# Kernel optimization log

Measured on AMD Instinct MI355X. Metric: run time of the kernel, lower is better.

Reference implementation:

```python
import jax, jax.numpy as jnp
import numpy as np

N_NODES = 10000
N_EDGES = 50000
N_GRAPHS = 64
NODE_DIM = 32
EDGE_DIM = 16
HID = 64
EDGE_HID = 128
OUT_DIM = 1
T_STEPS = 3       # message-passing rounds
S2S_STEPS = 6     # Set2Set processing steps


def setup_inputs() -> dict:
    key = jax.random.key(0)
    ks = jax.random.split(key, 24)
    def w(k, shape, scale):
        return (jax.random.normal(k, shape, dtype=jnp.float32) * scale)
    inp = {}
    inp["node_features"] = jax.random.normal(ks[0], (N_NODES, NODE_DIM), dtype=jnp.float32)
    inp["edge_features"] = jax.random.normal(ks[1], (N_EDGES, EDGE_DIM), dtype=jnp.float32)
    inp["edge_index"] = jax.random.randint(ks[2], (2, N_EDGES), 0, N_NODES, dtype=jnp.int32)
    # sorted, fully-covering graph assignment (nodes of each graph are contiguous)
    inp["batch_indices"] = ((jnp.arange(N_NODES) * N_GRAPHS) // N_NODES).astype(jnp.int32)
    # input projection
    inp["W_proj"] = w(ks[3], (NODE_DIM, HID), 1.0 / np.sqrt(NODE_DIM))
    inp["b_proj"] = jnp.zeros((HID,), jnp.float32)
    # edge network MLP: edge_dim -> edge_hid -> hid*hid
    inp["W_e1"] = w(ks[4], (EDGE_DIM, EDGE_HID), 1.0 / np.sqrt(EDGE_DIM))
    inp["b_e1"] = jnp.zeros((EDGE_HID,), jnp.float32)
    inp["W_e2"] = w(ks[5], (EDGE_HID, HID * HID), 0.01)
    inp["b_e2"] = jnp.zeros((HID * HID,), jnp.float32)
    # GRU cell (torch layout: 3*hid rows = r,z,n)
    inp["W_gih"] = w(ks[6], (3 * HID, HID), 1.0 / np.sqrt(HID))
    inp["W_ghh"] = w(ks[7], (3 * HID, HID), 1.0 / np.sqrt(HID))
    inp["b_gih"] = jnp.zeros((3 * HID,), jnp.float32)
    inp["b_ghh"] = jnp.zeros((3 * HID,), jnp.float32)
    # LSTM cell (torch layout: 4*hid rows = i,f,g,o), input 2*hid
    inp["W_lih"] = w(ks[8], (4 * HID, 2 * HID), 1.0 / np.sqrt(HID))
    inp["W_lhh"] = w(ks[9], (4 * HID, HID), 1.0 / np.sqrt(HID))
    inp["b_lih"] = jnp.zeros((4 * HID,), jnp.float32)
    inp["b_lhh"] = jnp.zeros((4 * HID,), jnp.float32)
    # readout MLP: 2*hid -> hid -> out
    inp["W_m1"] = w(ks[10], (2 * HID, HID), 1.0 / np.sqrt(2 * HID))
    inp["b_m1"] = jnp.zeros((HID,), jnp.float32)
    inp["W_m2"] = w(ks[11], (HID, OUT_DIM), 1.0 / np.sqrt(HID))
    inp["b_m2"] = jnp.zeros((OUT_DIM,), jnp.float32)
    return inp


def _scatter_softmax(e, idx, n_seg):
    mx = jax.ops.segment_max(e, idx, num_segments=n_seg)
    ex = jnp.exp(e - mx[idx])
    s = jax.ops.segment_sum(ex, idx, num_segments=n_seg)
    return ex / (s[idx] + 1e-16)


def _mpnn_forward(node_features, edge_features, edge_index, batch_indices,
                  W_proj, b_proj, W_e1, b_e1, W_e2, b_e2,
                  W_gih, W_ghh, b_gih, b_ghh,
                  W_lih, W_lhh, b_lih, b_lhh,
                  W_m1, b_m1, W_m2, b_m2):
    n_nodes = node_features.shape[0]
    dst = edge_index[0]  # receiving node v
    src = edge_index[1]  # sending node w

    # input projection
    h = node_features @ W_proj + b_proj                       # (N, H)

    # edge network: per-edge transformation matrix A(e_vw) (depends only on edge feats)
    A = jax.nn.relu(edge_features @ W_e1 + b_e1) @ W_e2 + b_e2
    A = A.reshape(-1, HID, HID)                               # (E, H, H)

    # T rounds: gather senders, per-edge bmm, scatter-add to receivers, GRU update
    for _ in range(T_STEPS):
        msgs = jnp.einsum('eij,ej->ei', A, h[src])            # (E, H)
        m = jax.ops.segment_sum(msgs, dst, num_segments=n_nodes)
        gx = m @ W_gih.T + b_gih                              # (N, 3H)
        gh = h @ W_ghh.T + b_ghh
        xr, xz, xn = jnp.split(gx, 3, axis=-1)
        hr, hz, hn = jnp.split(gh, 3, axis=-1)
        r = jax.nn.sigmoid(xr + hr)
        z = jax.nn.sigmoid(xz + hz)
        n = jnp.tanh(xn + r * hn)
        h = (1.0 - z) * n + z * h

    # Set2Set readout
    hs = jnp.zeros((N_GRAPHS, HID), h.dtype)
    cs = jnp.zeros((N_GRAPHS, HID), h.dtype)
    rs = jnp.zeros((N_GRAPHS, HID), h.dtype)
    for _ in range(S2S_STEPS):
        q = hs[batch_indices]                                 # (N, H)
        e = jnp.sum(h * q, axis=-1)                           # (N,)
        a = _scatter_softmax(e, batch_indices, N_GRAPHS)
        rs = jax.ops.segment_sum(a[:, None] * h, batch_indices, num_segments=N_GRAPHS)
        x = jnp.concatenate([hs, rs], axis=-1)                # (G, 2H)
        gates = x @ W_lih.T + b_lih + hs @ W_lhh.T + b_lhh    # (G, 4H)
        i, f, g, o = jnp.split(gates, 4, axis=-1)
        cs = jax.nn.sigmoid(f) * cs + jax.nn.sigmoid(i) * jnp.tanh(g)
        hs = jax.nn.sigmoid(o) * jnp.tanh(cs)
    ge = jnp.concatenate([hs, rs], axis=-1)                   # (G, 2H)
    return jax.nn.relu(ge @ W_m1 + b_m1) @ W_m2 + b_m2        # (G, out)


def reference(node_features, edge_features, edge_index, batch_indices,
              W_proj, b_proj, W_e1, b_e1, W_e2, b_e2,
              W_gih, W_ghh, b_gih, b_ghh,
              W_lih, W_lhh, b_lih, b_lhh,
              W_m1, b_m1, W_m2, b_m2):
    return _mpnn_forward(node_features, edge_features, edge_index, batch_indices,
                         W_proj, b_proj, W_e1, b_e1, W_e2, b_e2,
                         W_gih, W_ghh, b_gih, b_ghh,
                         W_lih, W_lhh, b_lih, b_lhh,
                         W_m1, b_m1, W_m2, b_m2)
```

## Files before the change

### kernel.cpp

```cpp
#include <hip/hip_runtime.h>

#define N_NODES   10000
#define N_EDGES   50000
#define N_GRAPHS  64
#define NODE_DIM  32
#define EDGE_DIM  16
#define HID       64
#define EHID      128
#define T_STEPS   3
#define S2S_STEPS 6

typedef _Float16 half_t;
typedef _Float16 f16x8 __attribute__((ext_vector_type(8)));
typedef float    f32x4 __attribute__((ext_vector_type(4)));

__device__ __forceinline__ float sigf(float x){ return 1.0f/(1.0f + expf(-x)); }

__global__ void k_zero(float* p, int n){
  int i = blockIdx.x*256 + threadIdx.x;
  if (i < n) p[i] = 0.0f;
}

__global__ void k_proj(const float* __restrict__ nf, const float* __restrict__ Wp,
                       const float* __restrict__ bp, float* __restrict__ h){
  int idx = blockIdx.x*256 + threadIdx.x;
  if (idx >= N_NODES*HID) return;
  int n = idx >> 6;
  int c = idx & 63;
  float acc = bp[c];
  const float* row = nf + (size_t)n*NODE_DIM;
  for (int j = 0; j < NODE_DIM; ++j)
    acc = fmaf(row[j], Wp[j*HID + c], acc);
  h[idx] = acc;
}

__global__ void k_tw2(const float* __restrict__ W2, float* __restrict__ Mm){
  int idx = blockIdx.x*256 + threadIdx.x;
  if (idx >= 64*8192) return;
  int j = idx >> 13; int o = idx & 8191; int k = o >> 6; int i = o & 63;
  Mm[idx] = W2[(size_t)k*4096 + i*64 + j];
}

__global__ void k_w2bt(const float* __restrict__ W2, half_t* __restrict__ BT){
  int idx = blockIdx.x*256 + threadIdx.x;
  if (idx >= 512*2*64*8) return;
  int j    = idx & 7;
  int lane = (idx >> 3) & 63;
  int tk   = (idx >> 9) & 1;
  int tn   = idx >> 10;
  int k = tk*32 + ((lane >> 4) << 3) + j;
  int o = tn*16 + (lane & 15);
  BT[idx] = (half_t)W2[(size_t)(o >> 6)*4096 + (o & 63)*64 + k];
}

__global__ void k_h2a(const float* __restrict__ h, half_t* __restrict__ AT){
  int idx = blockIdx.x*256 + threadIdx.x;
  if (idx >= 625*2*64*8) return;
  int j    = idx & 7;
  int lane = (idx >> 3) & 63;
  int tk   = (idx >> 9) & 1;
  int tm   = idx >> 10;
  int mrow = tm*16 + (lane & 15);
  int k    = tk*32 + ((lane >> 4) << 3) + j;
  AT[idx] = (half_t)h[(size_t)mrow*64 + k];
}

__global__ void k_prep(const float* __restrict__ h, const float* __restrict__ be2,
                       float* __restrict__ m, float* __restrict__ bhp,
                       half_t* __restrict__ AT){
  int idx = blockIdx.x*256 + threadIdx.x;
  if (idx >= N_NODES*HID) return;
  m[idx] = 0.0f;
  int n = idx >> 6, i = idx & 63;
  float acc = 0.0f;
  const float* row = be2 + (size_t)i*64;
  const float* hr  = h + (size_t)n*64;
  for (int j = 0; j < 64; ++j)
    acc = fmaf(row[j], hr[j], acc);
  bhp[idx] = acc;
  int j    = idx & 7;
  int lane = (idx >> 3) & 63;
  int tk   = (idx >> 9) & 1;
  int tm   = idx >> 10;
  int mrow = tm*16 + (lane & 15);
  int k    = tk*32 + ((lane >> 4) << 3) + j;
  AT[idx] = (half_t)h[(size_t)mrow*64 + k];
}

__global__ void k_twg(const float* __restrict__ Wg, const float* __restrict__ Wh,
                      float* __restrict__ WgT, float* __restrict__ WhT){
  int idx = blockIdx.x*256 + threadIdx.x;
  if (idx >= 192*64) return;
  int row = idx >> 6;
  int j   = idx & 63;
  WgT[j*192 + row] = Wg[(size_t)row*64 + j];
  WhT[j*192 + row] = Wh[(size_t)row*64 + j];
}

__global__ void k_ehid(const float* __restrict__ ef, const float* __restrict__ W1,
                       const float* __restrict__ b1, float* __restrict__ Hid){
  int idx = blockIdx.x*256 + threadIdx.x;
  if (idx >= N_EDGES*EHID) return;
  int e = idx >> 7, c = idx & 127;
  float acc = b1[c];
  const float* er = ef + (size_t)e*EDGE_DIM;
  for (int j = 0; j < EDGE_DIM; ++j)
    acc = fmaf(er[j], W1[j*EHID + c], acc);
  Hid[idx] = fmaxf(acc, 0.0f);
}

__global__ void k_ehid16(const float* __restrict__ ef, const float* __restrict__ W1,
                         const float* __restrict__ b1, half_t* __restrict__ Hid16){
  int idx = blockIdx.x*256 + threadIdx.x;
  if (idx >= N_EDGES*EHID) return;
  int e = idx >> 7, c = idx & 127;
  float acc = b1[c];
  const float* er = ef + (size_t)e*EDGE_DIM;
  for (int j = 0; j < EDGE_DIM; ++j)
    acc = fmaf(er[j], W1[j*EHID + c], acc);
  Hid16[idx] = (half_t)fmaxf(acc, 0.0f);
}

__global__ void k_bh(const float* __restrict__ h, const float* __restrict__ be2,
                     float* __restrict__ bh){
  int idx = blockIdx.x*256 + threadIdx.x;
  if (idx >= N_NODES*HID) return;
  int n = idx >> 6, i = idx & 63;
  float acc = 0.0f;
  const float* row = be2 + (size_t)i*64;
  const float* hr  = h + (size_t)n*64;
  for (int j = 0; j < 64; ++j)
    acc = fmaf(row[j], hr[j], acc);
  bh[idx] = acc;
}

__global__ void k_hist(const int* __restrict__ ei, int* __restrict__ deg){
  int e = blockIdx.x*256 + threadIdx.x;
  if (e >= N_EDGES) return;
  atomicAdd(&deg[ei[N_EDGES + e]], 1);
}

__global__ void k_scan(const int* __restrict__ deg, int* __restrict__ rowptr,
                       int* __restrict__ cursor){
  __shared__ int part[256];
  int t = threadIdx.x;
  int base = t*40;
  int s = 0;
  for (int i = 0; i < 40; ++i){
    int idx = base + i;
    if (idx < N_NODES) s += deg[idx];
  }
  part[t] = s;
  __syncthreads();
  for (int off = 1; off < 256; off <<= 1){
    int v = (t >= off) ? part[t - off] : 0;
    __syncthreads();
    part[t] += v;
    __syncthreads();
  }
  int run = (t > 0) ? part[t - 1] : 0;
  for (int i = 0; i < 40; ++i){
    int idx = base + i;
    if (idx < N_NODES){
      rowptr[idx] = run;
      cursor[idx] = run;
      run += deg[idx];
    }
  }
  if (t == 255) rowptr[N_NODES] = run;
}

__global__ void k_scatter(const int* __restrict__ ei, int* __restrict__ cursor,
                          int* __restrict__ csr){
  int e = blockIdx.x*256 + threadIdx.x;
  if (e >= N_EDGES) return;
  int src = ei[N_EDGES + e];
  int pos = atomicAdd(&cursor[src], 1);
  csr[pos] = e;
}

__global__ void MPNN_55705725829535_kernel(const half_t* __restrict__ AT,
                                           const half_t* __restrict__ BT,
                                           const int* __restrict__ rowptr,
                                           const int* __restrict__ csr,
                                           const int* __restrict__ ei,
                                           const half_t* __restrict__ Hid16,
                                           const float* __restrict__ bh,
                                           float* __restrict__ m){
  __shared__ half_t Ct[16][2][520];
  __shared__ int dstW[4][16];
  int wv   = threadIdx.x >> 6;
  int lane = threadIdx.x & 63;
  int quad = lane >> 4;
  int colb = lane & 15;
  int tm = blockIdx.x;
  int q  = blockIdx.y;
  int kh = blockIdx.z;

  const f16x8* Ab = (const f16x8*)AT + (size_t)tm*128;
  f16x8 a0 = Ab[lane];
  f16x8 a1 = Ab[64 + lane];
  #pragma unroll
  for (int ktl = 0; ktl < 2; ++ktl){
    int kt = kh*2 + ktl;
    f32x4 acc[8];
    #pragma unroll
    for (int jj = 0; jj < 8; ++jj){
      acc[jj][0]=0.f; acc[jj][1]=0.f; acc[jj][2]=0.f; acc[jj][3]=0.f;
    }
    #pragma unroll
    for (int jj = 0; jj < 8; ++jj){
      int ke = kt*32 + wv*8 + jj;
      int tn = ke*4 + q;
      const f16x8* Bb = (const f16x8*)BT + (size_t)tn*128;
      acc[jj] = __builtin_amdgcn_mfma_f32_16x16x32_f16(a0, Bb[lane],      acc[jj], 0, 0, 0);
      acc[jj] = __builtin_amdgcn_mfma_f32_16x16x32_f16(a1, Bb[64 + lane], acc[jj], 0, 0, 0);
    }
    #pragma unroll
    for (int r = 0; r < 4; ++r){
      int node = quad*4 + r;
      f16x8 v;
      #pragma unroll
      for (int jj = 0; jj < 8; ++jj) v[jj] = (half_t)acc[jj][r];
      *(f16x8*)&Ct[node][ktl][(wv*16 + colb)*8] = v;
    }
  }
  __syncthreads();

  for (int c = 0; c < 4; ++c){
    int node = wv*4 + c;
    int s = tm*16 + node;
    int beg  = rowptr[s];
    int endp = rowptr[s + 1];
    if (beg == endp) continue;
    f16x8 B0 = *(const f16x8*)&Ct[node][0][lane*8];
    f16x8 B1 = *(const f16x8*)&Ct[node][1][lane*8];
    float bhc = (kh == 0) ? bh[(size_t)s*64 + q*16 + colb] : 0.0f;
    for (int gbeg = beg; gbeg < endp; gbeg += 16){
      int gn = endp - gbeg; if (gn > 16) gn = 16;
      if (lane < 16)
        dstW[wv][lane] = (lane < gn) ? ei[csr[gbeg + lane]] : -1;
      f16x8 A0, A1;
      if (colb < gn){
        int e = csr[gbeg + colb];
        const f16x8* Hb = (const f16x8*)(Hid16 + (size_t)e*128) + quad;
        A0 = Hb[(kh*2 + 0)*4];
        A1 = Hb[(kh*2 + 1)*4];
      } else {
        #pragma unroll
        for (int p = 0; p < 8; ++p){ A0[p] = (half_t)0; A1[p] = (half_t)0; }
      }
      f32x4 acc;
      acc[0]=0.f; acc[1]=0.f; acc[2]=0.f; acc[3]=0.f;
      acc = __builtin_amdgcn_mfma_f32_16x16x32_f16(A0, B0, acc, 0, 0, 0);
      acc = __builtin_amdgcn_mfma_f32_16x16x32_f16(A1, B1, acc, 0, 0, 0);
      #pragma unroll
      for (int r = 0; r < 4; ++r){
        int jrow = quad*4 + r;
        if (jrow < gn){
          int d = dstW[wv][jrow];
          atomicAdd(&m[(size_t)d*64 + q*16 + colb], acc[r] + bhc);
        }
      }
    }
  }
}

__global__ void k_cgemm(const float* __restrict__ h, const float* __restrict__ Mm,
                        half_t* __restrict__ C, int lo, int hi){
  __shared__ float hs[16][64];
  int n0 = lo + blockIdx.x*16;
  int o0 = blockIdx.y*256 + threadIdx.x;
  for (int idx = threadIdx.x; idx < 16*64; idx += 256){
    int nn = idx >> 6, j = idx & 63;
    int node = n0 + nn;
    hs[nn][j] = (node < hi) ? h[(size_t)node*64 + j] : 0.0f;
  }
  __syncthreads();
  float acc0[16], acc1[16];
  #pragma unroll
  for (int nn = 0; nn < 16; ++nn){ acc0[nn] = 0.0f; acc1[nn] = 0.0f; }
  for (int j4 = 0; j4 < 16; ++j4){
    const float* M0 = Mm + (size_t)(j4*4)*8192;
    float a0 = M0[o0],            b0 = M0[o0 + 4096];
    float a1 = M0[8192 + o0],     b1 = M0[8192 + o0 + 4096];
    float a2 = M0[2*8192 + o0],   b2 = M0[2*8192 + o0 + 4096];
    float a3 = M0[3*8192 + o0],   b3 = M0[3*8192 + o0 + 4096];
    #pragma unroll
    for (int nn = 0; nn < 16; ++nn){
      float4 hv = *(const float4*)&hs[nn][j4*4];
      acc0[nn] = fmaf(hv.x, a0, acc0[nn]);
      acc1[nn] = fmaf(hv.x, b0, acc1[nn]);
      acc0[nn] = fmaf(hv.y, a1, acc0[nn]);
      acc1[nn] = fmaf(hv.y, b1, acc1[nn]);
      acc0[nn] = fmaf(hv.z, a2, acc0[nn]);
      acc1[nn] = fmaf(hv.z, b2, acc1[nn]);
      acc0[nn] = fmaf(hv.w, a3, acc0[nn]);
      acc1[nn] = fmaf(hv.w, b3, acc1[nn]);
    }
  }
  #pragma unroll
  for (int nn = 0; nn < 16; ++nn){
    int node = n0 + nn;
    if (node < hi){
      half_t* Cr = C + (size_t)(node - lo)*8192;
      Cr[o0]        = (half_t)acc0[nn];
      Cr[o0 + 4096] = (half_t)acc1[nn];
    }
  }
}

__global__ void k_msg_csr(const int* __restrict__ rowptr,
                          const int* __restrict__ csr,
                          const int* __restrict__ ei,
                          const float* __restrict__ Hid,
                          const half_t* __restrict__ C,
                          const float* __restrict__ bh,
                          float* __restrict__ m, int lo, int hi){
  __shared__ float hidL[4][8][128];
  int wave = threadIdx.x >> 6;
  int lane = threadIdx.x & 63;
  int s = lo + blockIdx.x*4 + wave;
  if (s >= hi) return;
  int beg = rowptr[s];
  int endp = rowptr[s + 1];
  if (beg == endp) return;
  float bhv = bh[(size_t)s*64 + lane];
  const half_t* Cb = C + (size_t)(s - lo)*8192 + lane;
  float (*hl)[128] = hidL[wave];
  for (int gbeg = beg; gbeg < endp; gbeg += 8){
    int gn = endp - gbeg; if (gn > 8) gn = 8;
    int dsts[8];
    int e0 = csr[gbeg];
    #pragma unroll
    for (int j = 0; j < 8; ++j){
      int e = (j < gn) ? csr[gbeg + j] : e0;
      dsts[j] = ei[e];
      hl[j][lane]      = Hid[(size_t)e*128 + lane];
      hl[j][lane + 64] = Hid[(size_t)e*128 + 64 + lane];
    }
    float acc[8];
    #pragma unroll
    for (int j = 0; j < 8; ++j) acc[j] = 0.0f;
    #pragma unroll 4
    for (int k = 0; k < 128; ++k){
      float c = (float)Cb[k*64];
      #pragma unroll
      for (int j = 0; j < 8; ++j)
        acc[j] = fmaf(hl[j][k], c, acc[j]);
    }
    for (int j = 0; j < gn; ++j)
      atomicAdd(&m[(size_t)dsts[j]*64 + lane], acc[j] + bhv);
  }
}

__global__ void k_msg_fb(const int* __restrict__ ei, const float* __restrict__ ef,
                         const float* __restrict__ W1, const float* __restrict__ b1,
                         const float* __restrict__ W2, const float* __restrict__ be2,
                         const float* __restrict__ h, float* __restrict__ m){
  __shared__ float HidL[EHID];
  __shared__ __align__(16) float hsL[HID];
  int e = blockIdx.x;
  int t = threadIdx.x;
  int src = ei[N_EDGES + e];
  int dst = ei[e];
  {
    float a0 = b1[t];
    float a1 = b1[t + 64];
    const float* er = ef + (size_t)e*EDGE_DIM;
    for (int j = 0; j < EDGE_DIM; ++j){
      float ev = er[j];
      a0 = fmaf(ev, W1[j*EHID + t],      a0);
      a1 = fmaf(ev, W1[j*EHID + t + 64], a1);
    }
    HidL[t]      = fmaxf(a0, 0.0f);
    HidL[t + 64] = fmaxf(a1, 0.0f);
    hsL[t] = h[(size_t)src*64 + t];
  }
  __syncthreads();
  float acc = 0.0f;
  for (int k = 0; k < EHID; ++k){
    float s = HidL[k];
    if (s != 0.0f){
      const float* w = W2 + (size_t)k*4096 + t*64;
      float partial = 0.0f;
      for (int j = 0; j < 64; ++j)
        partial = fmaf(hsL[j], w[j], partial);
      acc = fmaf(s, partial, acc);
    }
  }
  {
    const float* w = be2 + (size_t)t*64;
    for (int j = 0; j < 64; ++j)
      acc = fmaf(hsL[j], w[j], acc);
  }
  atomicAdd(&m[(size_t)dst*64 + t], acc);
}

__global__ void k_gru(float* __restrict__ h, const float* __restrict__ m,
                      const float* __restrict__ WgT, const float* __restrict__ WhT,
                      const float* __restrict__ bg, const float* __restrict__ bhb){
  __shared__ float mld[16][64];
  __shared__ float hld[16][64];
  int t  = threadIdx.x;
  int i  = t & 63;
  int wv = t >> 6;
  int n0 = blockIdx.x*16;
  for (int idx = t; idx < 16*64; idx += 256){
    int nn = idx >> 6, j = idx & 63;
    int node = n0 + nn;
    mld[nn][j] = m[(size_t)node*64 + j];
    hld[nn][j] = h[(size_t)node*64 + j];
  }
  __syncthreads();
  float xr[4], xz[4], xn[4], hr[4], hz[4], hn[4];
  #pragma unroll
  for (int c = 0; c < 4; ++c){
    xr[c] = bg[i];  xz[c] = bg[64 + i];  xn[c] = bg[128 + i];
    hr[c] = bhb[i]; hz[c] = bhb[64 + i]; hn[c] = bhb[128 + i];
  }
  for (int j = 0; j < 64; ++j){
    const float* wg = WgT + j*192;
    const float* wh = WhT + j*192;
    float wgr = wg[i], wgz = wg[64 + i], wgn = wg[128 + i];
    float whr = wh[i], whz = wh[64 + i], whn = wh[128 + i];
    #pragma unroll
    for (int c = 0; c < 4; ++c){
      int nn = wv*4 + c;
      float mj = mld[nn][j];
      float hj = hld[nn][j];
      xr[c] = fmaf(mj, wgr, xr[c]);
      xz[c] = fmaf(mj, wgz, xz[c]);
      xn[c] = fmaf(mj, wgn, xn[c]);
      hr[c] = fmaf(hj, whr, hr[c]);
      hz[c] = fmaf(hj, whz, hz[c]);
      hn[c] = fmaf(hj, whn, hn[c]);
    }
  }
  #pragma unroll
  for (int c = 0; c < 4; ++c){
    int nn = wv*4 + c;
    float r  = sigf(xr[c] + hr[c]);
    float z  = sigf(xz[c] + hz[c]);
    float nv = tanhf(xn[c] + r*hn[c]);
    h[(size_t)(n0 + nn)*64 + i] = (1.0f - z)*nv + z*hld[nn][i];
  }
}

__global__ void k_s2s(const float* __restrict__ h,
                      const float* __restrict__ Wli, const float* __restrict__ Wlh,
                      const float* __restrict__ bli, const float* __restrict__ blh,
                      const float* __restrict__ Wm1, const float* __restrict__ bm1,
                      const float* __restrict__ Wm2, const float* __restrict__ bm2,
                      float* __restrict__ out){
  __shared__ float hc[157*65];
  __shared__ float ea[160];
  __shared__ float x[192];
  __shared__ float gpart[512];
  __shared__ float rsp[8][64];
  __shared__ float wredA[8];
  __shared__ float wredB[8];
  __shared__ float hsb[64];
  __shared__ float csb[64];
  __shared__ float rsb[64];
  int g = blockIdx.x;
  int t = threadIdx.x;
  int lane = t & 63;
  int wv   = t >> 6;
  int start = (g*N_NODES + 63) >> 6;
  int end   = ((g + 1)*N_NODES + 63) >> 6;
  int cnt = end - start;
  const float* hg = h + (size_t)start*64;
  for (int idx = t; idx < cnt*64; idx += 512)
    hc[(idx >> 6)*65 + (idx & 63)] = hg[idx];
  if (t < 64){ hsb[t] = 0.0f; csb[t] = 0.0f; rsb[t] = 0.0f; }
  __syncthreads();
  for (int step = 0; step < S2S_STEPS; ++step){
    float ev = -1e30f;
    if (t < cnt){
      float a = 0.0f;
      const float* hr = &hc[t*65];
      for (int i = 0; i < 64; ++i) a = fmaf(hr[i], hsb[i], a);
      ev = a;
    }
    float v = ev;
    for (int o = 32; o > 0; o >>= 1) v = fmaxf(v, __shfl_xor(v, o));
    if (lane == 0) wredA[wv] = v;
    __syncthreads();
    float mx = wredA[0];
    #pragma unroll
    for (int i = 1; i < 8; ++i) mx = fmaxf(mx, wredA[i]);
    float ex = (t < cnt) ? expf(ev - mx) : 0.0f;
    float sv = ex;
    for (int o = 32; o > 0; o >>= 1) sv += __shfl_xor(sv, o);
    if (lane == 0) wredB[wv] = sv;
    __syncthreads();
    float ssum = 0.0f;
    #pragma unroll
    for (int i = 0; i < 8; ++i) ssum += wredB[i];
    if (t < cnt) ea[t] = ex / (ssum + 1e-16f);
    __syncthreads();
    {
      int n0 = wv*20;
      int n1 = n0 + 20; if (n1 > cnt) n1 = cnt;
      float r = 0.0f;
      for (int n = n0; n < n1; ++n)
        r = fmaf(ea[n], hc[n*65 + lane], r);
      rsp[wv][lane] = r;
    }
    __syncthreads();
    if (t < 64){
      float r = rsp[0][t] + rsp[1][t] + rsp[2][t] + rsp[3][t]
              + rsp[4][t] + rsp[5][t] + rsp[6][t] + rsp[7][t];
      rsb[t] = r;
      x[t]        = hsb[t];
      x[64 + t]   = r;
      x[128 + t]  = hsb[t];
    }
    __syncthreads();
    {
      int gate = t & 255;
      int half = t >> 8;
      float gl = 0.0f;
      if (half == 0){
        const float* wr = Wli + (size_t)gate*128;
        for (int jj = 0; jj < 96; ++jj) gl = fmaf(x[jj], wr[jj], gl);
      } else {
        const float* wr = Wli + (size_t)gate*128;
        for (int jj = 96; jj < 128; ++jj) gl = fmaf(x[jj], wr[jj], gl);
        const float* wh = Wlh + (size_t)gate*64;
        for (int jj = 0; jj < 64; ++jj) gl = fmaf(x[128 + jj], wh[jj], gl);
      }
      gpart[t] = gl;
    }
    __syncthreads();
    if (t < 64){
      float iv = sigf (gpart[t]       + gpart[t + 256]       + bli[t]       + blh[t]);
      float fv = sigf (gpart[64 + t]  + gpart[64 + t + 256]  + bli[64 + t]  + blh[64 + t]);
      float gv = tanhf(gpart[128 + t] + gpart[128 + t + 256] + bli[128 + t] + blh[128 + t]);
      float ov = sigf (gpart[192 + t] + gpart[192 + t + 256] + bli[192 + t] + blh[192 + t]);
      float c  = fv*csb[t] + iv*gv;
      csb[t] = c;
      hsb[t] = ov*tanhf(c);
    }
    __syncthreads();
  }
  float rv = 0.0f;
  if (t < 64){
    float v = bm1[t];
    for (int j = 0; j < 64; ++j) v = fmaf(hsb[j], Wm1[(size_t)j*64 + t],        v);
    for (int j = 0; j < 64; ++j) v = fmaf(rsb[j], Wm1[(size_t)(64 + j)*64 + t], v);
    v = fmaxf(v, 0.0f);
    rv = v * Wm2[t];
  }
  for (int o = 32; o > 0; o >>= 1) rv += __shfl_xor(rv, o);
  if (lane == 0) wredA[wv] = rv;
  __syncthreads();
  if (t == 0) out[g] = wredA[0] + wredA[1] + wredA[2] + wredA[3]
                     + wredA[4] + wredA[5] + wredA[6] + wredA[7] + bm2[0];
}

extern "C" void kernel_launch(void* const* d_in, const int* in_sizes, int n_in,
                              void* d_out, int out_size, void* d_ws, size_t ws_size,
                              hipStream_t stream){
  (void)in_sizes; (void)n_in; (void)out_size;

  const float* nf  = (const float*)d_in[0];
  const float* ef  = (const float*)d_in[1];
  const int*   ei  = (const int*)d_in[2];
  const float* Wp  = (const float*)d_in[4];
  const float* bp  = (const float*)d_in[5];
  const float* We1 = (const float*)d_in[6];
  const float* be1 = (const float*)d_in[7];
  const float* We2 = (const float*)d_in[8];
  const float* be2 = (const float*)d_in[9];
  const float* Wg  = (const float*)d_in[10];
  const float* Wh  = (const float*)d_in[11];
  const float* bg  = (const float*)d_in[12];
  const float* bhb = (const float*)d_in[13];
  const float* Wli = (const float*)d_in[14];
  const float* Wlh = (const float*)d_in[15];
  const float* bli = (const float*)d_in[16];
  const float* blh = (const float*)d_in[17];
  const float* Wm1 = (const float*)d_in[18];
  const float* bm1 = (const float*)d_in[19];
  const float* Wm2 = (const float*)d_in[20];
  const float* bm2 = (const float*)d_in[21];

  float* out = (float*)d_out;
  float* ws  = (float*)d_ws;

  float* h    = ws;
  float* m    = ws + 640000;
  float* bh   = ws + 1280000;
  float* Mm   = ws + 1920000;
  float* WgT  = ws + 2444288;
  float* WhT  = ws + 2456576;
  float* Hid  = ws + 2468864;
  half_t* Hid16 = (half_t*)Hid;
  int*   deg    = (int*)(ws + 8868864);
  int*   rowptr = deg + 10000;
  int*   cursor = rowptr + 10001;
  int*   csr    = cursor + 10000;
  half_t* AT  = (half_t*)(ws + 8948880);
  half_t* BT  = (half_t*)(ws + 9268880);
  const size_t C_OFF = 9531024;
  half_t* C   = (half_t*)(ws + C_OFF);

  long long c_halves = ((long long)ws_size - (long long)C_OFF*4) / 2;
  int NC = (c_halves > 0) ? (int)(c_halves / 8192) : 0;
  if (NC > N_NODES) NC = N_NODES;
  int use_c_path = (NC >= 512);
  int use_mfma   = (NC >= N_NODES);

  k_proj<<<(N_NODES*HID + 255)/256, 256, 0, stream>>>(nf, Wp, bp, h);

  if (use_c_path){
    k_twg <<<(192*64 + 255)/256, 256, 0, stream>>>(Wg, Wh, WgT, WhT);
    k_zero<<<(10000 + 255)/256, 256, 0, stream>>>((float*)deg, 10000);
    k_hist<<<(N_EDGES + 255)/256, 256, 0, stream>>>(ei, deg);
    k_scan<<<1, 256, 0, stream>>>(deg, rowptr, cursor);
    k_scatter<<<(N_EDGES + 255)/256, 256, 0, stream>>>(ei, cursor, csr);
    if (use_mfma){
      k_ehid16<<<(N_EDGES*EHID + 255)/256, 256, 0, stream>>>(ef, We1, be1, Hid16);
      k_w2bt<<<(512*2*64*8 + 255)/256, 256, 0, stream>>>(We2, BT);
      for (int step = 0; step < T_STEPS; ++step){
        k_prep<<<(N_NODES*HID + 255)/256, 256, 0, stream>>>(h, be2, m, bh, AT);
        dim3 grid(625, 4, 2);
        MPNN_55705725829535_kernel<<<grid, 256, 0, stream>>>(
            AT, BT, rowptr, csr, ei, Hid16, bh, m);
        k_gru<<<625, 256, 0, stream>>>(h, m, WgT, WhT, bg, bhb);
      }
    } else {
      k_ehid<<<(N_EDGES*EHID + 255)/256, 256, 0, stream>>>(ef, We1, be1, Hid);
      k_tw2<<<(64*8192)/256, 256, 0, stream>>>(We2, Mm);
      for (int step = 0; step < T_STEPS; ++step){
        k_zero<<<(N_NODES*HID + 255)/256, 256, 0, stream>>>(m, N_NODES*HID);
        k_bh<<<(N_NODES*HID + 255)/256, 256, 0, stream>>>(h, be2, bh);
        for (int lo = 0; lo < N_NODES; lo += NC){
          int hi = (lo + NC < N_NODES) ? lo + NC : N_NODES;
          int cnt = hi - lo;
          dim3 grid((cnt + 15)/16, 16);
          k_cgemm<<<grid, 256, 0, stream>>>(h, Mm, C, lo, hi);
          k_msg_csr<<<(cnt + 3)/4, 256, 0, stream>>>(
              rowptr, csr, ei, Hid, C, bh, m, lo, hi);
        }
        k_gru<<<625, 256, 0, stream>>>(h, m, WgT, WhT, bg, bhb);
      }
    }
  } else {
    k_twg <<<(192*64 + 255)/256, 256, 0, stream>>>(Wg, Wh, WgT, WhT);
    for (int step = 0; step < T_STEPS; ++step){
      k_zero<<<(N_NODES*HID + 255)/256, 256, 0, stream>>>(m, N_NODES*HID);
      k_msg_fb<<<N_EDGES, 64, 0, stream>>>(ei, ef, We1, be1, We2, be2, h, m);
      k_gru<<<625, 256, 0, stream>>>(h, m, WgT, WhT, bg, bhb);
    }
  }
  k_s2s<<<N_GRAPHS, 512, 0, stream>>>(h, Wli, Wlh, bli, blh,
                                      Wm1, bm1, Wm2, bm2, out);
}
```

Before: 580.8 us.

## Replace atomic message scatter with per-edge buffer and destination-CSR gather in GRU

New measurement: 622.0 us. 1.07x slower.

```diff
diff --git a/kernel.cpp b/kernel.cpp
--- a/kernel.cpp
+++ b/kernel.cpp
@@ -53,24 +53,10 @@
   BT[idx] = (half_t)W2[(size_t)(o >> 6)*4096 + (o & 63)*64 + k];
 }
 
-__global__ void k_h2a(const float* __restrict__ h, half_t* __restrict__ AT){
-  int idx = blockIdx.x*256 + threadIdx.x;
-  if (idx >= 625*2*64*8) return;
-  int j    = idx & 7;
-  int lane = (idx >> 3) & 63;
-  int tk   = (idx >> 9) & 1;
-  int tm   = idx >> 10;
-  int mrow = tm*16 + (lane & 15);
-  int k    = tk*32 + ((lane >> 4) << 3) + j;
-  AT[idx] = (half_t)h[(size_t)mrow*64 + k];
-}
-
 __global__ void k_prep(const float* __restrict__ h, const float* __restrict__ be2,
-                       float* __restrict__ m, float* __restrict__ bhp,
-                       half_t* __restrict__ AT){
+                       float* __restrict__ bhp, half_t* __restrict__ AT){
   int idx = blockIdx.x*256 + threadIdx.x;
   if (idx >= N_NODES*HID) return;
-  m[idx] = 0.0f;
   int n = idx >> 6, i = idx & 63;
   float acc = 0.0f;
   const float* row = be2 + (size_t)i*64;
@@ -134,10 +120,10 @@
   bh[idx] = acc;
 }
 
-__global__ void k_hist(const int* __restrict__ ei, int* __restrict__ deg){
+__global__ void k_hist(const int* __restrict__ ids, int* __restrict__ deg){
   int e = blockIdx.x*256 + threadIdx.x;
   if (e >= N_EDGES) return;
-  atomicAdd(&deg[ei[N_EDGES + e]], 1);
+  atomicAdd(&deg[ids[e]], 1);
 }
 
 __global__ void k_scan(const int* __restrict__ deg, int* __restrict__ rowptr,
@@ -170,12 +156,12 @@
   if (t == 255) rowptr[N_NODES] = run;
 }
 
-__global__ void k_scatter(const int* __restrict__ ei, int* __restrict__ cursor,
+__global__ void k_scatter(const int* __restrict__ ids, int* __restrict__ cursor,
                           int* __restrict__ csr){
   int e = blockIdx.x*256 + threadIdx.x;
   if (e >= N_EDGES) return;
-  int src = ei[N_EDGES + e];
-  int pos = atomicAdd(&cursor[src], 1);
+  int v = ids[e];
+  int pos = atomicAdd(&cursor[v], 1);
   csr[pos] = e;
 }
 
@@ -183,12 +169,11 @@
                                            const half_t* __restrict__ BT,
                                            const int* __restrict__ rowptr,
                                            const int* __restrict__ csr,
-                                           const int* __restrict__ ei,
                                            const half_t* __restrict__ Hid16,
                                            const float* __restrict__ bh,
-                                           float* __restrict__ m){
+                                           float* __restrict__ Msg){
   __shared__ half_t Ct[16][2][520];
-  __shared__ int dstW[4][16];
+  __shared__ int edgW[4][16];
   int wv   = threadIdx.x >> 6;
   int lane = threadIdx.x & 63;
   int quad = lane >> 4;
@@ -227,6 +212,7 @@
   }
   __syncthreads();
 
+  float* MsgK = Msg + (size_t)kh*(N_EDGES*64);
   for (int c = 0; c < 4; ++c){
     int node = wv*4 + c;
     int s = tm*16 + node;
@@ -239,10 +225,10 @@
     for (int gbeg = beg; gbeg < endp; gbeg += 16){
       int gn = endp - gbeg; if (gn > 16) gn = 16;
       if (lane < 16)
-        dstW[wv][lane] = (lane < gn) ? ei[csr[gbeg + lane]] : -1;
+        edgW[wv][lane] = (lane < gn) ? csr[gbeg + lane] : 0;
       f16x8 A0, A1;
       if (colb < gn){
-        int e = csr[gbeg + colb];
+        int e = edgW[wv][colb];
         const f16x8* Hb = (const f16x8*)(Hid16 + (size_t)e*128) + quad;
         A0 = Hb[(kh*2 + 0)*4];
         A1 = Hb[(kh*2 + 1)*4];
@@ -258,8 +244,8 @@
       for (int r = 0; r < 4; ++r){
         int jrow = quad*4 + r;
         if (jrow < gn){
-          int d = dstW[wv][jrow];
-          atomicAdd(&m[(size_t)d*64 + q*16 + colb], acc[r] + bhc);
+          int eid = edgW[wv][jrow];
+          MsgK[(size_t)eid*64 + q*16 + colb] = acc[r] + bhc;
         }
       }
     }
@@ -411,6 +397,64 @@
     int node = n0 + nn;
     mld[nn][j] = m[(size_t)node*64 + j];
     hld[nn][j] = h[(size_t)node*64 + j];
+  }
+  __syncthreads();
+  float xr[4], xz[4], xn[4], hr[4], hz[4], hn[4];
+  #pragma unroll
+  for (int c = 0; c < 4; ++c){
+    xr[c] = bg[i];  xz[c] = bg[64 + i];  xn[c] = bg[128 + i];
+    hr[c] = bhb[i]; hz[c] = bhb[64 + i]; hn[c] = bhb[128 + i];
+  }
+  for (int j = 0; j < 64; ++j){
+    const float* wg = WgT + j*192;
+    const float* wh = WhT + j*192;
+    float wgr = wg[i], wgz = wg[64 + i], wgn = wg[128 + i];
+    float whr = wh[i], whz = wh[64 + i], whn = wh[128 + i];
+    #pragma unroll
+    for (int c = 0; c < 4; ++c){
+      int nn = wv*4 + c;
+      float mj = mld[nn][j];
+      float hj = hld[nn][j];
+      xr[c] = fmaf(mj, wgr, xr[c]);
+      xz[c] = fmaf(mj, wgz, xz[c]);
+      xn[c] = fmaf(mj, wgn, xn[c]);
+      hr[c] = fmaf(hj, whr, hr[c]);
+      hz[c] = fmaf(hj, whz, hz[c]);
+      hn[c] = fmaf(hj, whn, hn[c]);
+    }
+  }
+  #pragma unroll
+  for (int c = 0; c < 4; ++c){
+    int nn = wv*4 + c;
+    float r  = sigf(xr[c] + hr[c]);
+    float z  = sigf(xz[c] + hz[c]);
+    float nv = tanhf(xn[c] + r*hn[c]);
+    h[(size_t)(n0 + nn)*64 + i] = (1.0f - z)*nv + z*hld[nn][i];
+  }
+}
+
+__global__ void k_gru2(float* __restrict__ h,
+                       const int* __restrict__ drow, const int* __restrict__ dcsr,
+                       const float* __restrict__ Msg,
+                       const float* __restrict__ WgT, const float* __restrict__ WhT,
+                       const float* __restrict__ bg, const float* __restrict__ bhb){
+  __shared__ float mld[16][64];
+  __shared__ float hld[16][64];
+  int t  = threadIdx.x;
+  int i  = t & 63;
+  int wv = t >> 6;
+  int n0 = blockIdx.x*16;
+  for (int idx = t; idx < 16*64; idx += 256){
+    int nn = idx >> 6, j = idx & 63;
+    int v = n0 + nn;
+    float acc = 0.0f;
+    int b = drow[v], e2 = drow[v + 1];
+    for (int p = b; p < e2; ++p){
+      size_t eo = (size_t)dcsr[p]*64 + j;
+      acc += Msg[eo] + Msg[(size_t)N_EDGES*64 + eo];
+    }
+    mld[nn][j] = acc;
+    hld[nn][j] = h[(size_t)v*64 + j];
   }
   __syncthreads();
   float xr[4], xz[4], xn[4], hr[4], hz[4], hn[4];
@@ -606,6 +650,11 @@
   half_t* BT  = (half_t*)(ws + 9268880);
   const size_t C_OFF = 9531024;
   half_t* C   = (half_t*)(ws + C_OFF);
+  int*   ddeg = (int*)(ws + C_OFF);
+  int*   drow = ddeg + 10000;
+  int*   dcur = drow + 10001;
+  int*   dcsr = dcur + 10000;
+  float* Msg  = ws + C_OFF + 80004;
 
   long long c_halves = ((long long)ws_size - (long long)C_OFF*4) / 2;
   int NC = (c_halves > 0) ? (int)(c_halves / 8192) : 0;
@@ -618,18 +667,22 @@
   if (use_c_path){
     k_twg <<<(192*64 + 255)/256, 256, 0, stream>>>(Wg, Wh, WgT, WhT);
     k_zero<<<(10000 + 255)/256, 256, 0, stream>>>((float*)deg, 10000);
-    k_hist<<<(N_EDGES + 255)/256, 256, 0, stream>>>(ei, deg);
+    k_hist<<<(N_EDGES + 255)/256, 256, 0, stream>>>(ei + N_EDGES, deg);
     k_scan<<<1, 256, 0, stream>>>(deg, rowptr, cursor);
-    k_scatter<<<(N_EDGES + 255)/256, 256, 0, stream>>>(ei, cursor, csr);
+    k_scatter<<<(N_EDGES + 255)/256, 256, 0, stream>>>(ei + N_EDGES, cursor, csr);
     if (use_mfma){
+      k_zero<<<(10000 + 255)/256, 256, 0, stream>>>((float*)ddeg, 10000);
+      k_hist<<<(N_EDGES + 255)/256, 256, 0, stream>>>(ei, ddeg);
+      k_scan<<<1, 256, 0, stream>>>(ddeg, drow, dcur);
+      k_scatter<<<(N_EDGES + 255)/256, 256, 0, stream>>>(ei, dcur, dcsr);
       k_ehid16<<<(N_EDGES*EHID + 255)/256, 256, 0, stream>>>(ef, We1, be1, Hid16);
       k_w2bt<<<(512*2*64*8 + 255)/256, 256, 0, stream>>>(We2, BT);
       for (int step = 0; step < T_STEPS; ++step){
-        k_prep<<<(N_NODES*HID + 255)/256, 256, 0, stream>>>(h, be2, m, bh, AT);
+        k_prep<<<(N_NODES*HID + 255)/256, 256, 0, stream>>>(h, be2, bh, AT);
         dim3 grid(625, 4, 2);
         MPNN_55705725829535_kernel<<<grid, 256, 0, stream>>>(
-            AT, BT, rowptr, csr, ei, Hid16, bh, m);
-        k_gru<<<625, 256, 0, stream>>>(h, m, WgT, WhT, bg, bhb);
+            AT, BT, rowptr, csr, Hid16, bh, Msg);
+        k_gru2<<<625, 256, 0, stream>>>(h, drow, dcsr, Msg, WgT, WhT, bg, bhb);
       }
     } else {
       k_ehid<<<(N_EDGES*EHID + 255)/256, 256, 0, stream>>>(ef, We1, be1, Hid);
```

## Batch five node tiles per block, keeping W2 fragments in registers across tiles

Applied to the files above, without the earlier changes.

Result: faster. 547.4 us (median of 3 runs) (-5.7%).

```diff
diff --git a/kernel.cpp b/kernel.cpp
--- a/kernel.cpp
+++ b/kernel.cpp
@@ -9,6 +9,7 @@
 #define EHID      128
 #define T_STEPS   3
 #define S2S_STEPS 6
+#define TMB       5
 
 typedef _Float16 half_t;
 typedef _Float16 f16x8 __attribute__((ext_vector_type(8)));
@@ -51,18 +52,6 @@
   int k = tk*32 + ((lane >> 4) << 3) + j;
   int o = tn*16 + (lane & 15);
   BT[idx] = (half_t)W2[(size_t)(o >> 6)*4096 + (o & 63)*64 + k];
-}
-
-__global__ void k_h2a(const float* __restrict__ h, half_t* __restrict__ AT){
-  int idx = blockIdx.x*256 + threadIdx.x;
-  if (idx >= 625*2*64*8) return;
-  int j    = idx & 7;
-  int lane = (idx >> 3) & 63;
-  int tk   = (idx >> 9) & 1;
-  int tm   = idx >> 10;
-  int mrow = tm*16 + (lane & 15);
-  int k    = tk*32 + ((lane >> 4) << 3) + j;
-  AT[idx] = (half_t)h[(size_t)mrow*64 + k];
 }
 
 __global__ void k_prep(const float* __restrict__ h, const float* __restrict__ be2,
@@ -134,10 +123,10 @@
   bh[idx] = acc;
 }
 
-__global__ void k_hist(const int* __restrict__ ei, int* __restrict__ deg){
+__global__ void k_hist(const int* __restrict__ ids, int* __restrict__ deg){
   int e = blockIdx.x*256 + threadIdx.x;
   if (e >= N_EDGES) return;
-  atomicAdd(&deg[ei[N_EDGES + e]], 1);
+  atomicAdd(&deg[ids[e]], 1);
 }
 
 __global__ void k_scan(const int* __restrict__ deg, int* __restrict__ rowptr,
@@ -170,99 +159,151 @@
   if (t == 255) rowptr[N_NODES] = run;
 }
 
-__global__ void k_scatter(const int* __restrict__ ei, int* __restrict__ cursor,
+__global__ void k_scatter(const int* __restrict__ ids, int* __restrict__ cursor,
                           int* __restrict__ csr){
   int e = blockIdx.x*256 + threadIdx.x;
   if (e >= N_EDGES) return;
-  int src = ei[N_EDGES + e];
-  int pos = atomicAdd(&cursor[src], 1);
+  int v = ids[e];
+  int pos = atomicAdd(&cursor[v], 1);
   csr[pos] = e;
 }
 
-__global__ void MPNN_55705725829535_kernel(const half_t* __restrict__ AT,
-                                           const half_t* __restrict__ BT,
-                                           const int* __restrict__ rowptr,
-                                           const int* __restrict__ csr,
-                                           const int* __restrict__ ei,
-                                           const half_t* __restrict__ Hid16,
-                                           const float* __restrict__ bh,
-                                           float* __restrict__ m){
+__global__ __launch_bounds__(256, 2)
+void MPNN_55705725829535_kernel(const half_t* __restrict__ AT,
+                                const half_t* __restrict__ BT,
+                                const int* __restrict__ rowptr,
+                                const int* __restrict__ csr,
+                                const int* __restrict__ ei,
+                                const half_t* __restrict__ Hid16,
+                                const float* __restrict__ bh,
+                                float* __restrict__ m){
   __shared__ half_t Ct[16][2][520];
-  __shared__ int dstW[4][16];
+  __shared__ int edgW[4][4][16];
+  __shared__ int dstW[4][4][16];
   int wv   = threadIdx.x >> 6;
   int lane = threadIdx.x & 63;
   int quad = lane >> 4;
   int colb = lane & 15;
-  int tm = blockIdx.x;
-  int q  = blockIdx.y;
-  int kh = blockIdx.z;
-
-  const f16x8* Ab = (const f16x8*)AT + (size_t)tm*128;
-  f16x8 a0 = Ab[lane];
-  f16x8 a1 = Ab[64 + lane];
+  int tmg = blockIdx.x;
+  int q   = blockIdx.y;
+  int kh  = blockIdx.z;
+
+  f16x8 B0r[2][8], B1r[2][8];
   #pragma unroll
-  for (int ktl = 0; ktl < 2; ++ktl){
-    int kt = kh*2 + ktl;
-    f32x4 acc[8];
+  for (int ktl = 0; ktl < 2; ++ktl)
     #pragma unroll
     for (int jj = 0; jj < 8; ++jj){
-      acc[jj][0]=0.f; acc[jj][1]=0.f; acc[jj][2]=0.f; acc[jj][3]=0.f;
-    }
+      int ke = (kh*2 + ktl)*32 + wv*8 + jj;
+      const f16x8* Bb = (const f16x8*)BT + (size_t)(ke*4 + q)*128;
+      B0r[ktl][jj] = Bb[lane];
+      B1r[ktl][jj] = Bb[64 + lane];
+    }
+
+  for (int tt = 0; tt < TMB; ++tt){
+    int tm = tmg*TMB + tt;
+    const f16x8* Ab = (const f16x8*)AT + (size_t)tm*128;
+    f16x8 a0 = Ab[lane];
+    f16x8 a1 = Ab[64 + lane];
+
+    {
+      int nodeL = wv*4 + quad;
+      int sL = tm*16 + nodeL;
+      int begL = rowptr[sL];
+      int endL = rowptr[sL + 1];
+      int eL = (colb < endL - begL) ? csr[begL + colb] : -1;
+      edgW[wv][quad][colb] = eL;
+      dstW[wv][quad][colb] = (eL >= 0) ? ei[eL] : -1;
+    }
+
     #pragma unroll
-    for (int jj = 0; jj < 8; ++jj){
-      int ke = kt*32 + wv*8 + jj;
-      int tn = ke*4 + q;
-      const f16x8* Bb = (const f16x8*)BT + (size_t)tn*128;
-      acc[jj] = __builtin_amdgcn_mfma_f32_16x16x32_f16(a0, Bb[lane],      acc[jj], 0, 0, 0);
-      acc[jj] = __builtin_amdgcn_mfma_f32_16x16x32_f16(a1, Bb[64 + lane], acc[jj], 0, 0, 0);
-    }
-    #pragma unroll
-    for (int r = 0; r < 4; ++r){
-      int node = quad*4 + r;
-      f16x8 v;
+    for (int ktl = 0; ktl < 2; ++ktl){
+      f32x4 acc[8];
       #pragma unroll
-      for (int jj = 0; jj < 8; ++jj) v[jj] = (half_t)acc[jj][r];
-      *(f16x8*)&Ct[node][ktl][(wv*16 + colb)*8] = v;
-    }
-  }
-  __syncthreads();
-
-  for (int c = 0; c < 4; ++c){
-    int node = wv*4 + c;
-    int s = tm*16 + node;
-    int beg  = rowptr[s];
-    int endp = rowptr[s + 1];
-    if (beg == endp) continue;
-    f16x8 B0 = *(const f16x8*)&Ct[node][0][lane*8];
-    f16x8 B1 = *(const f16x8*)&Ct[node][1][lane*8];
-    float bhc = (kh == 0) ? bh[(size_t)s*64 + q*16 + colb] : 0.0f;
-    for (int gbeg = beg; gbeg < endp; gbeg += 16){
-      int gn = endp - gbeg; if (gn > 16) gn = 16;
-      if (lane < 16)
-        dstW[wv][lane] = (lane < gn) ? ei[csr[gbeg + lane]] : -1;
-      f16x8 A0, A1;
-      if (colb < gn){
-        int e = csr[gbeg + colb];
-        const f16x8* Hb = (const f16x8*)(Hid16 + (size_t)e*128) + quad;
-        A0 = Hb[(kh*2 + 0)*4];
-        A1 = Hb[(kh*2 + 1)*4];
-      } else {
-        #pragma unroll
-        for (int p = 0; p < 8; ++p){ A0[p] = (half_t)0; A1[p] = (half_t)0; }
+      for (int jj = 0; jj < 8; ++jj){
+        acc[jj][0]=0.f; acc[jj][1]=0.f; acc[jj][2]=0.f; acc[jj][3]=0.f;
       }
-      f32x4 acc;
-      acc[0]=0.f; acc[1]=0.f; acc[2]=0.f; acc[3]=0.f;
-      acc = __builtin_amdgcn_mfma_f32_16x16x32_f16(A0, B0, acc, 0, 0, 0);
-      acc = __builtin_amdgcn_mfma_f32_16x16x32_f16(A1, B1, acc, 0, 0, 0);
+      #pragma unroll
+      for (int jj = 0; jj < 8; ++jj){
+        acc[jj] = __builtin_amdgcn_mfma_f32_16x16x32_f16(a0, B0r[ktl][jj], acc[jj], 0, 0, 0);
+        acc[jj] = __builtin_amdgcn_mfma_f32_16x16x32_f16(a1, B1r[ktl][jj], acc[jj], 0, 0, 0);
+      }
       #pragma unroll
       for (int r = 0; r < 4; ++r){
-        int jrow = quad*4 + r;
-        if (jrow < gn){
-          int d = dstW[wv][jrow];
-          atomicAdd(&m[(size_t)d*64 + q*16 + colb], acc[r] + bhc);
+        int node = quad*4 + r;
+        f16x8 v;
+        #pragma unroll
+        for (int jj = 0; jj < 8; ++jj) v[jj] = (half_t)acc[jj][r];
+        *(f16x8*)&Ct[node][ktl][(wv*16 + colb)*8] = v;
+      }
+    }
+    __syncthreads();
+
+    for (int c = 0; c < 4; ++c){
+      int node = wv*4 + c;
+      int s = tm*16 + node;
+      int beg  = rowptr[s];
+      int endp = rowptr[s + 1];
+      if (beg == endp) continue;
+      f16x8 B0 = *(const f16x8*)&Ct[node][0][lane*8];
+      f16x8 B1 = *(const f16x8*)&Ct[node][1][lane*8];
+      float bhc = (kh == 0) ? bh[(size_t)s*64 + q*16 + colb] : 0.0f;
+      int gn0 = endp - beg; if (gn0 > 16) gn0 = 16;
+      {
+        f16x8 A0, A1;
+        int e = (colb < gn0) ? edgW[wv][c][colb] : -1;
+        if (e >= 0){
+          const f16x8* Hb = (const f16x8*)(Hid16 + (size_t)e*128) + quad;
+          A0 = Hb[(kh*2 + 0)*4];
+          A1 = Hb[(kh*2 + 1)*4];
+        } else {
+          #pragma unroll
+          for (int p = 0; p < 8; ++p){ A0[p] = (half_t)0; A1[p] = (half_t)0; }
+        }
+        f32x4 acc;
+        acc[0]=0.f; acc[1]=0.f; acc[2]=0.f; acc[3]=0.f;
+        acc = __builtin_amdgcn_mfma_f32_16x16x32_f16(A0, B0, acc, 0, 0, 0);
+        acc = __builtin_amdgcn_mfma_f32_16x16x32_f16(A1, B1, acc, 0, 0, 0);
+        #pragma unroll
+        for (int r = 0; r < 4; ++r){
+          int jrow = quad*4 + r;
+          if (jrow < gn0){
+            int d = dstW[wv][c][jrow];
+            atomicAdd(&m[(size_t)d*64 + q*16 + colb], acc[r] + bhc);
+          }
         }
       }
-    }
+      for (int gbeg = beg + 16; gbeg < endp; gbeg += 16){
+        int gn = endp - gbeg; if (gn > 16) gn = 16;
+        if (lane < 16){
+          int e2 = (lane < gn) ? csr[gbeg + lane] : -1;
+          edgW[wv][c][lane] = e2;
+          dstW[wv][c][lane] = (e2 >= 0) ? ei[e2] : -1;
+        }
+        f16x8 A0, A1;
+        int e = (colb < gn) ? edgW[wv][c][colb] : -1;
+        if (e >= 0){
+          const f16x8* Hb = (const f16x8*)(Hid16 + (size_t)e*128) + quad;
+          A0 = Hb[(kh*2 + 0)*4];
+          A1 = Hb[(kh*2 + 1)*4];
+        } else {
+          #pragma unroll
+          for (int p = 0; p < 8; ++p){ A0[p] = (half_t)0; A1[p] = (half_t)0; }
+        }
+        f32x4 acc;
+        acc[0]=0.f; acc[1]=0.f; acc[2]=0.f; acc[3]=0.f;
+        acc = __builtin_amdgcn_mfma_f32_16x16x32_f16(A0, B0, acc, 0, 0, 0);
+        acc = __builtin_amdgcn_mfma_f32_16x16x32_f16(A1, B1, acc, 0, 0, 0);
+        #pragma unroll
+        for (int r = 0; r < 4; ++r){
+          int jrow = quad*4 + r;
+          if (jrow < gn){
+            int d = dstW[wv][c][jrow];
+            atomicAdd(&m[(size_t)d*64 + q*16 + colb], acc[r] + bhc);
+          }
+        }
+      }
+    }
+    __syncthreads();
   }
 }
 
@@ -618,15 +659,15 @@
   if (use_c_path){
     k_twg <<<(192*64 + 255)/256, 256, 0, stream>>>(Wg, Wh, WgT, WhT);
     k_zero<<<(10000 + 255)/256, 256, 0, stream>>>((float*)deg, 10000);
-    k_hist<<<(N_EDGES + 255)/256, 256, 0, stream>>>(ei, deg);
+    k_hist<<<(N_EDGES + 255)/256, 256, 0, stream>>>(ei + N_EDGES, deg);
     k_scan<<<1, 256, 0, stream>>>(deg, rowptr, cursor);
-    k_scatter<<<(N_EDGES + 255)/256, 256, 0, stream>>>(ei, cursor, csr);
+    k_scatter<<<(N_EDGES + 255)/256, 256, 0, stream>>>(ei + N_EDGES, cursor, csr);
     if (use_mfma){
       k_ehid16<<<(N_EDGES*EHID + 255)/256, 256, 0, stream>>>(ef, We1, be1, Hid16);
       k_w2bt<<<(512*2*64*8 + 255)/256, 256, 0, stream>>>(We2, BT);
       for (int step = 0; step < T_STEPS; ++step){
         k_prep<<<(N_NODES*HID + 255)/256, 256, 0, stream>>>(h, be2, m, bh, AT);
-        dim3 grid(625, 4, 2);
+        dim3 grid(625/TMB, 4, 2);
         MPNN_55705725829535_kernel<<<grid, 256, 0, stream>>>(
             AT, BT, rowptr, csr, ei, Hid16, bh, m);
         k_gru<<<625, 256, 0, stream>>>(h, m, WgT, WhT, bg, bhb);
```
